# Kernel tuning notes

Hardware: AMD Instinct MI355X
Metric: run time of the kernel (lower is better)

The kernel has to match this reference:

```python
import jax, jax.numpy as jnp
import numpy as np

RES = 64
CHANNEL = 32
DIM = 512
BATCH = 32


def setup_inputs() -> dict:
    key = jax.random.key(0)
    k_style, k_U, k_L, k_mu = jax.random.split(key, 4)
    style = jax.random.normal(k_style, (BATCH, DIM), dtype=jnp.float32)
    U = jax.random.normal(k_U, (RES, RES, CHANNEL, DIM), dtype=jnp.float32)
    L = jax.random.normal(k_L, (DIM,), dtype=jnp.float32)
    mu = jax.random.normal(k_mu, (RES, RES, CHANNEL), dtype=jnp.float32)
    return {"style": style, "U": U, "L": L, "mu": mu}


def reference(style, U, L, mu):
    # temp = U[None] * (L * style)[:, None, None, None, :]; h = temp.sum(-1) + mu
    # Fused as a contraction over dim d: out[b,r,s,c] = sum_d U[r,s,c,d] * L[d] * style[b,d]
    scaled = L[None, :] * style  # [batch, dim]
    h = jnp.einsum('rscd,bd->brsc', U, scaled) + mu[None, :, :, :]
    return h
```

## Files before the change

kernel.cpp:

```cpp
#include <hip/hip_runtime.h>

#define RES 64
#define CHANNEL 32
#define DIM 512
#define BATCH 32
#define ROWS (RES * RES * CHANNEL)

__global__ void scale_kernel(const float* __restrict__ style,
                             const float* __restrict__ L,
                             float* __restrict__ scaledT) {
    int i = blockIdx.x * 256 + threadIdx.x;
    int d = i >> 5;
    int b = i & 31;
    scaledT[i] = L[d] * style[b * DIM + d];
}

__global__ __launch_bounds__(256, 2) void eigen_kernel(
    const float* __restrict__ U,
    const float* __restrict__ mu,
    const float* __restrict__ scaledT,
    float* __restrict__ out) {

    __shared__ __align__(16) float Sc[DIM * BATCH];

    const int tid = threadIdx.x;

    {
        const float4* g = (const float4*)scaledT;
        float4* s = (float4*)Sc;
#pragma unroll
        for (int j = 0; j < 16; ++j)
            s[j * 256 + tid] = g[j * 256 + tid];
    }
    __syncthreads();

    const size_t row = (size_t)blockIdx.x * 256 + tid;
    const float4* __restrict__ u4 = (const float4*)(U + row * DIM);
    const float4* __restrict__ sc4 = (const float4*)Sc;

    float acc[BATCH];
#pragma unroll
    for (int b = 0; b < BATCH; ++b) acc[b] = 0.0f;

    float4 cur[4], nxt[4];
#pragma unroll
    for (int p = 0; p < 4; ++p) cur[p] = u4[p];

#pragma unroll 1
    for (int body = 0; body < DIM / 16; ++body) {
        if (body + 1 < DIM / 16) {
#pragma unroll
            for (int p = 0; p < 4; ++p) nxt[p] = u4[(body + 1) * 4 + p];
        }
#pragma unroll
        for (int p = 0; p < 4; ++p) {
            const int dbase = body * 16 + p * 4;
#pragma unroll
            for (int j = 0; j < 4; ++j) {
                const float uj = (j == 0) ? cur[p].x : (j == 1) ? cur[p].y
                               : (j == 2) ? cur[p].z : cur[p].w;
                const int sbase = (dbase + j) * 8;
#pragma unroll
                for (int q = 0; q < 8; ++q) {
                    float4 s = sc4[sbase + q];
                    acc[q * 4 + 0] += uj * s.x;
                    acc[q * 4 + 1] += uj * s.y;
                    acc[q * 4 + 2] += uj * s.z;
                    acc[q * 4 + 3] += uj * s.w;
                }
            }
        }
#pragma unroll
        for (int p = 0; p < 4; ++p) cur[p] = nxt[p];
    }

    const float muv = mu[row];
#pragma unroll
    for (int b = 0; b < BATCH; ++b)
        out[(size_t)b * ROWS + row] = acc[b] + muv;
}

extern "C" void kernel_launch(void* const* d_in, const int* in_sizes, int n_in,
                              void* d_out, int out_size, void* d_ws, size_t ws_size,
                              hipStream_t stream) {
    const float* style = (const float*)d_in[0];
    const float* U     = (const float*)d_in[1];
    const float* L     = (const float*)d_in[2];
    const float* mu    = (const float*)d_in[3];
    float* out = (float*)d_out;
    float* scaledT = (float*)d_ws;

    scale_kernel<<<64, 256, 0, stream>>>(style, L, scaledT);
    eigen_kernel<<<ROWS / 256, 256, 0, stream>>>(U, mu, scaledT, out);
}
```

Measured before the change: 387.1 us.

## Compute contraction with bf16 split-precision MFMA instead of scalar FP32 FMAs

Replaces the per-thread scalar FP32 FMA loop over an LDS-staged scale table with wave-level 16x16x32 bf16 MFMA instructions. Both U and the scaled style are split into hi/lo bf16 pairs (three-term product) to approximate FP32 accuracy. The scale table is pre-packed into an MFMA operand layout read directly from global memory, removing the shared-memory stage. This targets the compute-bound FMA throughput at the cost of in-loop conversion work and slightly reduced precision.

```diff
diff --git a/kernel.cpp b/kernel.cpp
--- a/kernel.cpp
+++ b/kernel.cpp
@@ -6,78 +6,125 @@
 #define BATCH 32
 #define ROWS (RES * RES * CHANNEL)
 
-__global__ void scale_kernel(const float* __restrict__ style,
-                             const float* __restrict__ L,
-                             float* __restrict__ scaledT) {
+typedef unsigned short u16;
+typedef float f32x4v __attribute__((ext_vector_type(4)));
+typedef short bf16x8 __attribute__((ext_vector_type(8)));
+
+__device__ __forceinline__ uint32_t bf16_rne_bits(float x) {
+    uint32_t u = __float_as_uint(x);
+    return u + 0x7fffu + ((u >> 16) & 1u);
+}
+
+__global__ void scale_pack_kernel(const float* __restrict__ style,
+                                  const float* __restrict__ L,
+                                  u16* __restrict__ tab) {
     int i = blockIdx.x * 256 + threadIdx.x;
     int d = i >> 5;
     int b = i & 31;
-    scaledT[i] = L[d] * style[b * DIM + d];
+    float s = L[d] * style[b * DIM + d];
+    uint32_t t = bf16_rne_bits(s);
+    u16 hi = (u16)(t >> 16);
+    float hf = __uint_as_float(t & 0xffff0000u);
+    float lf = s - hf;
+    u16 lo = (u16)(bf16_rne_bits(lf) >> 16);
+
+    int kc = d >> 5, kg = (d >> 3) & 3, j = d & 7;
+    int nt = b >> 4, lc = b & 15;
+    int base = kc * 2048 + nt * 1024 + (kg * 16 + lc) * 8 + j;
+    tab[base]       = hi;
+    tab[base + 512] = lo;
 }
 
-__global__ __launch_bounds__(256, 2) void eigen_kernel(
+__device__ __forceinline__ void cvt_hl(const float4& p, const float4& q,
+                                       bf16x8& h, bf16x8& l) {
+    float x[8] = {p.x, p.y, p.z, p.w, q.x, q.y, q.z, q.w};
+#pragma unroll
+    for (int j = 0; j < 8; ++j) {
+        uint32_t t = bf16_rne_bits(x[j]);
+        h[j] = (short)(t >> 16);
+        float hf = __uint_as_float(t & 0xffff0000u);
+        l[j] = (short)(bf16_rne_bits(x[j] - hf) >> 16);
+    }
+}
+
+__global__ __launch_bounds__(256) void eigen_mfma_kernel(
     const float* __restrict__ U,
     const float* __restrict__ mu,
-    const float* __restrict__ scaledT,
+    const u16* __restrict__ tab,
     float* __restrict__ out) {
 
-    __shared__ __align__(16) float Sc[DIM * BATCH];
+    const int tid  = threadIdx.x;
+    const int wid  = tid >> 6;
+    const int lane = tid & 63;
+    const int lc   = lane & 15;
+    const int kg   = lane >> 4;
 
-    const int tid = threadIdx.x;
+    const int m0 = blockIdx.x * 128 + wid * 32;
 
-    {
-        const float4* g = (const float4*)scaledT;
-        float4* s = (float4*)Sc;
-#pragma unroll
-        for (int j = 0; j < 16; ++j)
-            s[j * 256 + tid] = g[j * 256 + tid];
-    }
-    __syncthreads();
+    const float4* __restrict__ a0 = (const float4*)(U + (size_t)(m0 + lc) * DIM + kg * 8);
+    const float4* __restrict__ a1 = (const float4*)(U + (size_t)(m0 + 16 + lc) * DIM + kg * 8);
+    const u16* __restrict__ bp = tab + lane * 8;
 
-    const size_t row = (size_t)blockIdx.x * 256 + tid;
-    const float4* __restrict__ u4 = (const float4*)(U + row * DIM);
-    const float4* __restrict__ sc4 = (const float4*)Sc;
+    f32x4v acc00 = {0.f, 0.f, 0.f, 0.f};
+    f32x4v acc01 = acc00;
+    f32x4v acc10 = acc00;
+    f32x4v acc11 = acc00;
 
-    float acc[BATCH];
-#pragma unroll
-    for (int b = 0; b < BATCH; ++b) acc[b] = 0.0f;
-
-    float4 cur[4], nxt[4];
-#pragma unroll
-    for (int p = 0; p < 4; ++p) cur[p] = u4[p];
+    float4 c0a = a0[0], c0b = a0[1], c1a = a1[0], c1b = a1[1];
+    bf16x8 bh0 = *(const bf16x8*)(bp);
+    bf16x8 bl0 = *(const bf16x8*)(bp + 512);
+    bf16x8 bh1 = *(const bf16x8*)(bp + 1024);
+    bf16x8 bl1 = *(const bf16x8*)(bp + 1536);
 
 #pragma unroll 1
-    for (int body = 0; body < DIM / 16; ++body) {
-        if (body + 1 < DIM / 16) {
-#pragma unroll
-            for (int p = 0; p < 4; ++p) nxt[p] = u4[(body + 1) * 4 + p];
+    for (int kc = 0; kc < DIM / 32; ++kc) {
+        float4 n0a, n0b, n1a, n1b;
+        bf16x8 nh0, nl0, nh1, nl1;
+        if (kc < 15) {
+            const int o = (kc + 1) * 8;
+            n0a = a0[o];     n0b = a0[o + 1];
+            n1a = a1[o];     n1b = a1[o + 1];
+            const u16* nb = bp + (kc + 1) * 2048;
+            nh0 = *(const bf16x8*)(nb);
+            nl0 = *(const bf16x8*)(nb + 512);
+            nh1 = *(const bf16x8*)(nb + 1024);
+            nl1 = *(const bf16x8*)(nb + 1536);
         }
-#pragma unroll
-        for (int p = 0; p < 4; ++p) {
-            const int dbase = body * 16 + p * 4;
-#pragma unroll
-            for (int j = 0; j < 4; ++j) {
-                const float uj = (j == 0) ? cur[p].x : (j == 1) ? cur[p].y
-                               : (j == 2) ? cur[p].z : cur[p].w;
-                const int sbase = (dbase + j) * 8;
-#pragma unroll
-                for (int q = 0; q < 8; ++q) {
-                    float4 s = sc4[sbase + q];
-                    acc[q * 4 + 0] += uj * s.x;
-                    acc[q * 4 + 1] += uj * s.y;
-                    acc[q * 4 + 2] += uj * s.z;
-                    acc[q * 4 + 3] += uj * s.w;
-                }
-            }
+
+        bf16x8 uh0, ul0, uh1, ul1;
+        cvt_hl(c0a, c0b, uh0, ul0);
+        cvt_hl(c1a, c1b, uh1, ul1);
+
+        acc00 = __builtin_amdgcn_mfma_f32_16x16x32_bf16(bh0, uh0, acc00, 0, 0, 0);
+        acc10 = __builtin_amdgcn_mfma_f32_16x16x32_bf16(bh0, uh1, acc10, 0, 0, 0);
+        acc01 = __builtin_amdgcn_mfma_f32_16x16x32_bf16(bh1, uh0, acc01, 0, 0, 0);
+        acc11 = __builtin_amdgcn_mfma_f32_16x16x32_bf16(bh1, uh1, acc11, 0, 0, 0);
+        acc00 = __builtin_amdgcn_mfma_f32_16x16x32_bf16(bl0, uh0, acc00, 0, 0, 0);
+        acc10 = __builtin_amdgcn_mfma_f32_16x16x32_bf16(bl0, uh1, acc10, 0, 0, 0);
+        acc01 = __builtin_amdgcn_mfma_f32_16x16x32_bf16(bl1, uh0, acc01, 0, 0, 0);
+        acc11 = __builtin_amdgcn_mfma_f32_16x16x32_bf16(bl1, uh1, acc11, 0, 0, 0);
+        acc00 = __builtin_amdgcn_mfma_f32_16x16x32_bf16(bh0, ul0, acc00, 0, 0, 0);
+        acc10 = __builtin_amdgcn_mfma_f32_16x16x32_bf16(bh0, ul1, acc10, 0, 0, 0);
+        acc01 = __builtin_amdgcn_mfma_f32_16x16x32_bf16(bh1, ul0, acc01, 0, 0, 0);
+        acc11 = __builtin_amdgcn_mfma_f32_16x16x32_bf16(bh1, ul1, acc11, 0, 0, 0);
+
+        if (kc < 15) {
+            c0a = n0a; c0b = n0b; c1a = n1a; c1b = n1b;
+            bh0 = nh0; bl0 = nl0; bh1 = nh1; bl1 = nl1;
         }
-#pragma unroll
-        for (int p = 0; p < 4; ++p) cur[p] = nxt[p];
     }
 
-    const float muv = mu[row];
+    const float mu0 = mu[m0 + lc];
+    const float mu1 = mu[m0 + 16 + lc];
+    const size_t col0 = (size_t)(m0 + lc);
+    const size_t col1 = (size_t)(m0 + 16 + lc);
 #pragma unroll
-    for (int b = 0; b < BATCH; ++b)
-        out[(size_t)b * ROWS + row] = acc[b] + muv;
+    for (int r = 0; r < 4; ++r) {
+        out[(size_t)(kg * 4 + r) * ROWS + col0]        = acc00[r] + mu0;
+        out[(size_t)(kg * 4 + r) * ROWS + col1]        = acc10[r] + mu1;
+        out[(size_t)(16 + kg * 4 + r) * ROWS + col0]   = acc01[r] + mu0;
+        out[(size_t)(16 + kg * 4 + r) * ROWS + col1]   = acc11[r] + mu1;
+    }
 }
 
 extern "C" void kernel_launch(void* const* d_in, const int* in_sizes, int n_in,
@@ -88,8 +135,8 @@
     const float* L     = (const float*)d_in[2];
     const float* mu    = (const float*)d_in[3];
     float* out = (float*)d_out;
-    float* scaledT = (float*)d_ws;
+    u16* tab = (u16*)d_ws;
 
-    scale_kernel<<<64, 256, 0, stream>>>(style, L, scaledT);
-    eigen_kernel<<<ROWS / 256, 256, 0, stream>>>(U, mu, scaledT, out);
+    scale_pack_kernel<<<64, 256, 0, stream>>>(style, L, tab);
+    eigen_mfma_kernel<<<ROWS / 128, 256, 0, stream>>>(U, mu, tab, out);
 }
```

New measurement: 381.0 us. About the same (-1.6%).
